# Kernel tuning notes

Hardware: AMD Instinct MI355X
Metric: run time of the kernel (lower is better)

## Reference

```python
import jax, jax.numpy as jnp
import numpy as np

DIM = 1024
N_HEADS = 16
HEAD_DIM = DIM // N_HEADS  # 64
HALF = HEAD_DIM // 2       # 32
DEPTH = 6
N_BRANCH = 2
NEG_INF = -1e9


def _rot_H(x, cos, sin, m):
    # H direction: adjacent-pair complex layout (..., HALF, 2)
    # x: [B,S,H,D], cos/sin: [HALF], m: [B,S] int
    B, S, H, D = x.shape
    xr = x.reshape(B, S, H, HALF, 2)
    re, im = xr[..., 0], xr[..., 1]
    re2 = re * cos - im * sin
    im2 = re * sin + im * cos
    rot = jnp.stack([re2, im2], axis=-1).reshape(B, S, H, D)
    return jnp.where((m != 0)[:, :, None, None], rot, x)


def _rot_B(x, cos, sin, m):
    # B direction: split-half complex layout (real = first half, imag = second half)
    re, im = x[..., :HALF], x[..., HALF:]
    re2 = re * cos - im * sin
    im2 = re * sin + im * cos
    rot = jnp.concatenate([re2, im2], axis=-1)
    return jnp.where((m != 0)[:, :, None, None], rot, x)


def _apply_rope_instructions(x, H_mask, B_mask, freqs_cos, freqs_sin):
    # Sequentially compose rotations per depth level, as in the torch loops.
    for i in range(DEPTH):
        x = _rot_H(x, freqs_cos[1], freqs_sin[1], H_mask[i])
        for b in range(N_BRANCH):
            x = _rot_B(x, freqs_cos[b + 1], freqs_sin[b + 1], B_mask[i, b])
    return x


def setup_inputs() -> dict:
    key = jax.random.key(0)
    ks = jax.random.split(key, 10)
    B, S = 2, 1024
    x = jax.random.normal(ks[0], (B, S, DIM), dtype=jnp.float32)
    masks = jax.random.randint(ks[1], (B, 1, S, S), 0, 2, dtype=jnp.int32)
    H_mask = jax.random.randint(ks[2], (DEPTH, B, S), 0, 2, dtype=jnp.int32)
    B_mask = jax.random.randint(ks[3], (DEPTH, N_BRANCH, B, S), 0, 2, dtype=jnp.int32)
    theta = jax.random.uniform(ks[4], (4, HALF), dtype=jnp.float32) * 2.0 * np.pi
    freqs_cos = jnp.cos(theta)
    freqs_sin = jnp.sin(theta)
    scale = 1.0 / np.sqrt(DIM)
    wq = jax.random.normal(ks[5], (DIM, DIM), dtype=jnp.float32) * scale
    wk = jax.random.normal(ks[6], (DIM, DIM), dtype=jnp.float32) * scale
    wv = jax.random.normal(ks[7], (DIM, DIM), dtype=jnp.float32) * scale
    wo = jax.random.normal(ks[8], (DIM, DIM), dtype=jnp.float32) * scale
    return {"x": x, "masks": masks, "H_mask": H_mask, "B_mask": B_mask,
            "freqs_cos": freqs_cos, "freqs_sin": freqs_sin,
            "wq": wq, "wk": wk, "wv": wv, "wo": wo}


def reference(x, masks, H_mask, B_mask, freqs_cos, freqs_sin, wq, wk, wv, wo):
    B, S, _ = x.shape
    xq = (x @ wq).reshape(B, S, N_HEADS, HEAD_DIM)
    xk = (x @ wk).reshape(B, S, N_HEADS, HEAD_DIM)
    xv = (x @ wv).reshape(B, S, N_HEADS, HEAD_DIM)
    xq = _apply_rope_instructions(xq, H_mask, B_mask, freqs_cos, freqs_sin)
    xk = _apply_rope_instructions(xk, H_mask, B_mask, freqs_cos, freqs_sin)
    scores = jnp.einsum('bqhd,bkhd->bhqk', xq, xk) / np.sqrt(HEAD_DIM)
    scores = jnp.where(masks == 0, NEG_INF, scores)
    probs = jax.nn.softmax(scores, axis=-1)
    out = jnp.einsum('bhqk,bkhd->bqhd', probs, xv).reshape(B, S, DIM)
    return out @ wo
```

## Files before the change

### kernel.cpp

```cpp
#include <hip/hip_runtime.h>

#define SLEN 1024
#define BATCH 2
#define DEPTH 6

typedef _Float16 h8 __attribute__((ext_vector_type(8)));
typedef float    f4 __attribute__((ext_vector_type(4)));
#define MF16(a, b, c) __builtin_amdgcn_mfma_f32_16x16x32_f16(a, b, c, 0, 0, 0)

#define SW(row, c) ((((c) ^ ((row) & 7))) * 8)

__device__ __forceinline__ void async_cp16(const _Float16* g, _Float16* l) {
  __builtin_amdgcn_global_load_lds(
      (const __attribute__((address_space(1))) void*)g,
      (__attribute__((address_space(3))) void*)l, 16, 0, 0);
}

__global__ __launch_bounds__(256) void prep(const float* __restrict__ x,
    const float* __restrict__ wq, const float* __restrict__ wk,
    const float* __restrict__ wv, const float* __restrict__ wo,
    const int* __restrict__ masks, _Float16* __restrict__ xh,
    _Float16* __restrict__ qt, _Float16* __restrict__ kt,
    _Float16* __restrict__ vt, _Float16* __restrict__ ot,
    unsigned int* __restrict__ mpk) {
  __shared__ _Float16 T[64][72];
  const int bid = blockIdx.x, t = threadIdx.x;
  if (bid < 1024) {
    int idx = (bid * 256 + t) * 8;
    float4 f0 = *(const float4*)(x + idx);
    float4 f1 = *(const float4*)(x + idx + 4);
    union { h8 v; _Float16 e[8]; } u;
    u.e[0] = (_Float16)f0.x; u.e[1] = (_Float16)f0.y;
    u.e[2] = (_Float16)f0.z; u.e[3] = (_Float16)f0.w;
    u.e[4] = (_Float16)f1.x; u.e[5] = (_Float16)f1.y;
    u.e[6] = (_Float16)f1.z; u.e[7] = (_Float16)f1.w;
    *(h8*)(xh + idx) = u.v;
  } else if (bid < 2048) {
    const int i = bid - 1024;
    const int wsel = i >> 8;
    const float* W = wsel == 0 ? wq : wsel == 1 ? wk : wsel == 2 ? wv : wo;
    _Float16* O = wsel == 0 ? qt : wsel == 1 ? kt : wsel == 2 ? vt : ot;
    const int k0 = ((i >> 4) & 15) * 64, n0 = (i & 15) * 64;
    const int rr = t >> 2, cs = (t & 3) * 16;
    #pragma unroll
    for (int j = 0; j < 4; ++j) {
      float4 f = *(const float4*)(W + (size_t)(k0 + rr) * 1024 + n0 + cs + j * 4);
      T[rr][cs + j * 4 + 0] = (_Float16)f.x;
      T[rr][cs + j * 4 + 1] = (_Float16)f.y;
      T[rr][cs + j * 4 + 2] = (_Float16)f.z;
      T[rr][cs + j * 4 + 3] = (_Float16)f.w;
    }
    __syncthreads();
    const int n = t >> 2, ks = (t & 3) * 16;
    union { h8 v; _Float16 e[8]; } u0, u1;
    #pragma unroll
    for (int j = 0; j < 8; ++j) { u0.e[j] = T[ks + j][n]; u1.e[j] = T[ks + 8 + j][n]; }
    *(h8*)(O + (size_t)(n0 + n) * 1024 + k0 + ks)     = u0.v;
    *(h8*)(O + (size_t)(n0 + n) * 1024 + k0 + ks + 8) = u1.v;
  } else {
    const int g = (bid - 2048) * 256 + t;
    const int row = g >> 5, w = g & 31;
    const int* m = masks + (size_t)row * 1024 + w * 32;
    unsigned int bits = 0;
    #pragma unroll
    for (int j4 = 0; j4 < 8; ++j4) {
      int4 mm = *(const int4*)(m + j4 * 4);
      if (mm.x) bits |= 1u << (j4 * 4 + 0);
      if (mm.y) bits |= 1u << (j4 * 4 + 1);
      if (mm.z) bits |= 1u << (j4 * 4 + 2);
      if (mm.w) bits |= 1u << (j4 * 4 + 3);
    }
    mpk[g] = bits;
  }
}

template <int TMODE, typename CT>
__device__ __forceinline__ void gemm16(const _Float16* __restrict__ A,
                                       const _Float16* __restrict__ Bt,
                                       CT* __restrict__ C,
                                       const int* __restrict__ Hm,
                                       const int* __restrict__ Bm,
                                       _Float16* __restrict__ SH,
                                       const float* __restrict__ FR) {
  _Float16* As = SH;
  _Float16* Bs = SH + 4096;
  const int t    = threadIdx.x;
  const int bm   = blockIdx.y * 64, bn = blockIdx.x * 128;
  const int w    = t >> 6, lane = t & 63;
  const int ln15 = lane & 15, quad = lane >> 4;
  const int wm   = (w >> 1) * 32, wn = (w & 1) * 64;

  const int srow8 = lane >> 3;
  const int sch   = (lane & 7) ^ srow8;
  const _Float16* agp = A  + (size_t)(bm + w * 16 + srow8) * 1024 + sch * 8;
  const _Float16* bgp = Bt + (size_t)(bn + w * 32 + srow8) * 1024 + sch * 8;

  f4 acc[2][4];
  #pragma unroll
  for (int i = 0; i < 2; ++i)
    #pragma unroll
    for (int j = 0; j < 4; ++j) acc[i][j] = (f4){0.f, 0.f, 0.f, 0.f};

  for (int k0 = 0; k0 < 1024; k0 += 64) {
    #pragma unroll
    for (int j = 0; j < 2; ++j)
      async_cp16(agp + k0 + j * 8192, As + w * 1024 + j * 512);
    #pragma unroll
    for (int j = 0; j < 4; ++j)
      async_cp16(bgp + k0 + j * 8192, Bs + w * 2048 + j * 512);
    __syncthreads();
    #pragma unroll
    for (int kk = 0; kk < 8; kk += 4) {
      h8 af[2], bf[4];
      #pragma unroll
      for (int i = 0; i < 2; ++i) {
        int row = wm + i * 16 + ln15;
        af[i] = *(const h8*)&As[row * 64 + SW(row, kk + quad)];
      }
      #pragma unroll
      for (int j = 0; j < 4; ++j) {
        int row = wn + j * 16 + ln15;
        bf[j] = *(const h8*)&Bs[row * 64 + SW(row, kk + quad)];
      }
      #pragma unroll
      for (int i = 0; i < 2; ++i)
        #pragma unroll
        for (int j = 0; j < 4; ++j)
          acc[i][j] = MF16(af[i], bf[j], acc[i][j]);
    }
    __syncthreads();
  }

  if (TMODE == 0) {
    #pragma unroll
    for (int i = 0; i < 2; ++i) {
      int row = bm + wm + i * 16 + quad * 4;
      #pragma unroll
      for (int r = 0; r < 4; ++r)
        #pragma unroll
        for (int j = 0; j < 4; ++j)
          C[(size_t)(row + r) * 1024 + bn + wn + j * 16 + ln15] = (CT)acc[i][j][r];
    }
  } else if (TMODE == 1) {
    #pragma unroll
    for (int i = 0; i < 2; ++i) {
      int m0 = bm + wm + i * 16 + quad * 4;
      #pragma unroll
      for (int r = 0; r < 4; ++r) {
        int m = m0 + r;
        size_t base = ((size_t)(m >> 10) * 1024) * 1024 + (m & 1023);
        #pragma unroll
        for (int j = 0; j < 4; ++j)
          C[base + (size_t)(bn + wn + j * 16 + ln15) * 1024] = (CT)acc[i][j][r];
      }
    }
  } else {
    _Float16* EP = SH;
    #pragma unroll
    for (int i = 0; i < 2; ++i)
      #pragma unroll
      for (int j = 0; j < 4; ++j) {
        int cl = wn + j * 16 + ln15;
        #pragma unroll
        for (int r = 0; r < 4; ++r) {
          int rl = wm + i * 16 + quad * 4 + r;
          EP[rl * 128 + (((cl >> 3) ^ (rl & 15)) << 3) + (cl & 7)] =
              (_Float16)acc[i][j][r];
        }
      }
    __syncthreads();
    const int row = t >> 2, head = (t >> 1) & 1, p = t & 1;
    const int bs = bm + row;
    const int r15 = row & 15;
    float vv[32];
    #pragma unroll
    for (int cc = 0; cc < 4; ++cc) {
      int lc = head * 8 + 2 * p + (cc & 1) + (cc >> 1) * 4;
      union { h8 v; _Float16 e[8]; } u;
      u.v = *(const h8*)&EP[row * 128 + (lc ^ r15) * 8];
      #pragma unroll
      for (int e = 0; e < 8; ++e) vv[cc * 8 + e] = (float)u.e[e];
    }
    #pragma unroll 1
    for (int d = 0; d < DEPTH; ++d) {
      if (Hm[d * (BATCH * SLEN) + bs] != 0) {
        #pragma unroll
        for (int jj = 0; jj < 8; ++jj) {
          int j0 = 8 * p + jj, j1 = 16 + 8 * p + jj;
          float re0 = vv[2 * jj], im0 = vv[2 * jj + 1];
          vv[2 * jj]     = re0 * FR[j0] - im0 * FR[32 + j0];
          vv[2 * jj + 1] = re0 * FR[32 + j0] + im0 * FR[j0];
          float re1 = vv[16 + 2 * jj], im1 = vv[17 + 2 * jj];
          vv[16 + 2 * jj] = re1 * FR[j1] - im1 * FR[32 + j1];
          vv[17 + 2 * jj] = re1 * FR[32 + j1] + im1 * FR[j1];
        }
      }
      if (Bm[(d * 2 + 0) * (BATCH * SLEN) + bs] != 0) {
        #pragma unroll
        for (int jj = 0; jj < 16; ++jj) {
          int j = 16 * p + jj;
          float re = vv[jj], im = vv[16 + jj];
          vv[jj]      = re * FR[j] - im * FR[32 + j];
          vv[16 + jj] = re * FR[32 + j] + im * FR[j];
        }
      }
      if (Bm[(d * 2 + 1) * (BATCH * SLEN) + bs] != 0) {
        #pragma unroll
        for (int jj = 0; jj < 16; ++jj) {
          int j = 16 * p + jj;
          float re = vv[jj], im = vv[16 + jj];
          vv[jj]      = re * FR[64 + j] - im * FR[96 + j];
          vv[16 + jj] = re * FR[96 + j] + im * FR[64 + j];
        }
      }
    }
    _Float16* dst = (_Float16*)C + (size_t)(bm + row) * 1024 + bn + head * 64;
    #pragma unroll
    for (int cc = 0; cc < 4; ++cc) {
      union { h8 v; _Float16 e[8]; } u;
      #pragma unroll
      for (int e = 0; e < 8; ++e) u.e[e] = (_Float16)vv[cc * 8 + e];
      int off = (cc < 2) ? (16 * p + cc * 8) : (32 + 16 * p + (cc - 2) * 8);
      *(h8*)(dst + off) = u.v;
    }
  }
}

__global__ __launch_bounds__(256) void gemm_qkv16(
    const _Float16* __restrict__ xh, const _Float16* __restrict__ qt,
    const _Float16* __restrict__ kt, const _Float16* __restrict__ vtw,
    _Float16* __restrict__ q, _Float16* __restrict__ k,
    _Float16* __restrict__ vth, const int* __restrict__ Hm,
    const int* __restrict__ Bm, const float* __restrict__ fc,
    const float* __restrict__ fs) {
  __shared__ _Float16 SH[12288];
  __shared__ float FR[128];
  if (blockIdx.z != 2 && threadIdx.x < 128) {
    int g = threadIdx.x & 31;
    FR[threadIdx.x] = (threadIdx.x < 32) ? fc[32 + g]
                    : (threadIdx.x < 64) ? fs[32 + g]
                    : (threadIdx.x < 96) ? fc[64 + g] : fs[64 + g];
  }
  if (blockIdx.z == 2)
    gemm16<1, _Float16>(xh, vtw, vth, nullptr, nullptr, SH, nullptr);
  else if (blockIdx.z == 1)
    gemm16<2, _Float16>(xh, kt, k, Hm, Bm, SH, FR);
  else
    gemm16<2, _Float16>(xh, qt, q, Hm, Bm, SH, FR);
}

__global__ __launch_bounds__(256) void gemm_o16(
    const _Float16* __restrict__ A, const _Float16* __restrict__ Bt,
    float* __restrict__ C) {
  __shared__ _Float16 SH[12288];
  gemm16<0, float>(A, Bt, C, nullptr, nullptr, SH, nullptr);
}

__global__ __launch_bounds__(256) void attn_mfma(const _Float16* __restrict__ qh,
    const _Float16* __restrict__ kh, const _Float16* __restrict__ vth,
    const unsigned int* __restrict__ mpk, _Float16* __restrict__ out) {
  __shared__ _Float16 Ks[2][64 * 64];
  __shared__ _Float16 Vs[2][64 * 64];
  __shared__ _Float16 QP[4][16][72];

  const int t    = threadIdx.x;
  const int w    = t >> 6, lane = t & 63;
  const int ln15 = lane & 15, quad = lane >> 4;

  const int bh = blockIdx.x & 31;
  const int s0 = (blockIdx.x >> 5) * 64;
  const int b = bh >> 4, h = bh & 15;
  const size_t qkbase = (size_t)b * (SLEN * 1024) + h * 64;
  const size_t vbase  = ((size_t)b * 1024 + h * 64) * SLEN;

  {
    const int srow = t >> 2, sc0 = (t & 3) * 16;
    const _Float16* src = qh + qkbase + (size_t)(s0 + srow) * 1024 + sc0;
    *(h8*)&QP[w][srow & 15][sc0]     = *(const h8*)src;
    *(h8*)&QP[w][srow & 15][sc0 + 8] = *(const h8*)(src + 8);
  }
  h8 aq0 = *(h8*)&QP[w][ln15][quad * 8];
  h8 aq1 = *(h8*)&QP[w][ln15][32 + quad * 8];

  const int srow8 = lane >> 3;
  const int sch   = (lane & 7) ^ srow8;
  const _Float16* kgp = kh + qkbase + (size_t)(w * 16 + srow8) * 1024 + sch * 8;
  const _Float16* vgp = vth + vbase + (size_t)(w * 16 + srow8) * 1024 + sch * 8;

  const unsigned int* mp = mpk + ((size_t)b * SLEN + s0 + w * 16 + quad * 4) * 32;

  float lrow[4] = {1e-30f, 1e-30f, 1e-30f, 1e-30f};
  f4 oacc[4];
  #pragma unroll
  for (int f = 0; f < 4; ++f) oacc[f] = (f4){0.f, 0.f, 0.f, 0.f};

  async_cp16(kgp,        &Ks[0][w * 1024]);
  async_cp16(kgp + 8192, &Ks[0][w * 1024 + 512]);
  async_cp16(vgp,        &Vs[0][w * 1024]);
  async_cp16(vgp + 8192, &Vs[0][w * 1024 + 512]);
  unsigned int w0[4], w1[4];
  #pragma unroll
  for (int r = 0; r < 4; ++r) { w0[r] = mp[r * 32]; w1[r] = mp[r * 32 + 1]; }
  __syncthreads();

  for (int c = 0; c < 16; ++c) {
    const int cur = c & 1;
    unsigned int nw0[4], nw1[4];
    if (c < 15) {
      const size_t ko = (size_t)((c + 1) * 64) * 1024;
      const int    vo = (c + 1) * 64;
      async_cp16(kgp + ko,        &Ks[cur ^ 1][w * 1024]);
      async_cp16(kgp + ko + 8192, &Ks[cur ^ 1][w * 1024 + 512]);
      async_cp16(vgp + vo,        &Vs[cur ^ 1][w * 1024]);
      async_cp16(vgp + vo + 8192, &Vs[cur ^ 1][w * 1024 + 512]);
      #pragma unroll
      for (int r = 0; r < 4; ++r) {
        nw0[r] = mp[r * 32 + (c + 1) * 2];
        nw1[r] = mp[r * 32 + (c + 1) * 2 + 1];
      }
    }

    f4 s[4];
    #pragma unroll
    for (int f = 0; f < 4; ++f) {
      int row = f * 16 + ln15;
      h8 bk0 = *(const h8*)&Ks[cur][row * 64 + SW(row, quad)];
      h8 bk1 = *(const h8*)&Ks[cur][row * 64 + SW(row, 4 + quad)];
      f4 acc = (f4){0.f, 0.f, 0.f, 0.f};
      acc = MF16(aq0, bk0, acc);
      acc = MF16(aq1, bk1, acc);
      s[f] = acc;
    }
    #pragma unroll
    for (int f = 0; f < 4; ++f) {
      const int col = f * 16 + ln15;
      #pragma unroll
      for (int r = 0; r < 4; ++r) {
        unsigned int wd = (col & 32) ? w1[r] : w0[r];
        float p = ((wd >> (col & 31)) & 1u)
                    ? __expf(s[f][r] * 0.125f - 3.0f) : 0.0f;
        lrow[r] += p;
        QP[w][quad * 4 + r][col] = (_Float16)p;
      }
    }
    h8 ap0 = *(h8*)&QP[w][ln15][quad * 8];
    h8 ap1 = *(h8*)&QP[w][ln15][32 + quad * 8];
    #pragma unroll
    for (int f = 0; f < 4; ++f) {
      int row = f * 16 + ln15;
      h8 bv0 = *(const h8*)&Vs[cur][row * 64 + SW(row, quad)];
      h8 bv1 = *(const h8*)&Vs[cur][row * 64 + SW(row, 4 + quad)];
      f4 o = oacc[f];
      o = MF16(ap0, bv0, o);
      o = MF16(ap1, bv1, o);
      oacc[f] = o;
    }
    if (c < 15) {
      #pragma unroll
      for (int r = 0; r < 4; ++r) { w0[r] = nw0[r]; w1[r] = nw1[r]; }
    }
    __syncthreads();
  }

  #pragma unroll
  for (int r = 0; r < 4; ++r) {
    float sm = lrow[r];
    sm += __shfl_xor(sm, 1);
    sm += __shfl_xor(sm, 2);
    sm += __shfl_xor(sm, 4);
    sm += __shfl_xor(sm, 8);
    lrow[r] = 1.0f / sm;
  }
  #pragma unroll
  for (int f = 0; f < 4; ++f)
    #pragma unroll
    for (int r = 0; r < 4; ++r)
      QP[w][quad * 4 + r][f * 16 + ln15] = (_Float16)(oacc[f][r] * lrow[r]);
  const int orow = lane >> 2, oseg = (lane & 3) * 16;
  _Float16* op = out + qkbase + (size_t)(s0 + w * 16 + orow) * 1024 + oseg;
  *(h8*)op       = *(h8*)&QP[w][orow][oseg];
  *(h8*)(op + 8) = *(h8*)&QP[w][orow][oseg + 8];
}

extern "C" void kernel_launch(void* const* d_in, const int* in_sizes, int n_in,
                              void* d_out, int out_size, void* d_ws, size_t ws_size,
                              hipStream_t stream) {
  const float* x     = (const float*)d_in[0];
  const int*   masks = (const int*)d_in[1];
  const int*   Hm    = (const int*)d_in[2];
  const int*   Bm    = (const int*)d_in[3];
  const float* fc    = (const float*)d_in[4];
  const float* fs    = (const float*)d_in[5];
  const float* wq    = (const float*)d_in[6];
  const float* wk    = (const float*)d_in[7];
  const float* wv    = (const float*)d_in[8];
  const float* wo    = (const float*)d_in[9];
  float* out = (float*)d_out;

  _Float16* xh   = (_Float16*)d_ws;
  _Float16* wqt  = xh + (1 << 21);
  _Float16* wkt  = wqt + (1 << 20);
  _Float16* wvt  = wkt + (1 << 20);
  _Float16* wot  = wvt + (1 << 20);
  _Float16* qhh  = wot + (1 << 20);
  _Float16* khh  = qhh + (1 << 21);
  _Float16* vth  = khh + (1 << 21);
  _Float16* aoh  = vth + (1 << 21);
  unsigned int* mpk = (unsigned int*)(aoh + (1 << 21));

  dim3 blk(256);
  prep<<<dim3(2304), blk, 0, stream>>>(x, wq, wk, wv, wo, masks,
                                       xh, wqt, wkt, wvt, wot, mpk);
  gemm_qkv16<<<dim3(8, 32, 3), blk, 0, stream>>>(xh, wqt, wkt, wvt,
                                                 qhh, khh, vth, Hm, Bm, fc, fs);
  attn_mfma<<<dim3(512), blk, 0, stream>>>(qhh, khh, vth, mpk, aoh);
  gemm_o16<<<dim3(8, 32), blk, 0, stream>>>(aoh, wot, out);
}
```

Before: 158.9 us.

## Switch attention to 32x32 MFMA with 2x2 wave split over query and key halves

Rewrites the attention kernel's inner loop to use 32x32x16 MFMA instead of 16x16x32. The four waves are arranged as a 2x2 grid over query-row halves and key-column halves, and the partial outputs and row sums are combined through LDS at the end. The aim is fewer MFMA issues and fewer LDS fragment loads per tile, plus better operand reuse. In exchange it adds a cross-wave reduction epilogue with extra LDS traffic and syncs, and each wave now holds 16 mask words in registers.

Result: slower. 163.1 us (+2.6%).

```diff
diff --git a/kernel.cpp b/kernel.cpp
--- a/kernel.cpp
+++ b/kernel.cpp
@@ -6,7 +6,9 @@
 
 typedef _Float16 h8 __attribute__((ext_vector_type(8)));
 typedef float    f4 __attribute__((ext_vector_type(4)));
+typedef float    f16f __attribute__((ext_vector_type(16)));
 #define MF16(a, b, c) __builtin_amdgcn_mfma_f32_16x16x32_f16(a, b, c, 0, 0, 0)
+#define MF32(a, b, c) __builtin_amdgcn_mfma_f32_32x32x16_f16(a, b, c, 0, 0, 0)
 
 #define SW(row, c) ((((c) ^ ((row) & 7))) * 8)
 
@@ -259,13 +261,15 @@
 __global__ __launch_bounds__(256) void attn_mfma(const _Float16* __restrict__ qh,
     const _Float16* __restrict__ kh, const _Float16* __restrict__ vth,
     const unsigned int* __restrict__ mpk, _Float16* __restrict__ out) {
-  __shared__ _Float16 Ks[2][64 * 64];
-  __shared__ _Float16 Vs[2][64 * 64];
-  __shared__ _Float16 QP[4][16][72];
+  __shared__ _Float16 Ks[2][4096];
+  __shared__ _Float16 Vs[2][4096];
+  __shared__ _Float16 PB[4][1280];
 
   const int t    = threadIdx.x;
   const int w    = t >> 6, lane = t & 63;
-  const int ln15 = lane & 15, quad = lane >> 4;
+  const int l31  = lane & 31, hh = lane >> 5;
+  const int qh32 = (w & 1) * 32;
+  const int kh32 = (w >> 1) * 32;
 
   const int bh = blockIdx.x & 31;
   const int s0 = (blockIdx.x >> 5) * 64;
@@ -274,38 +278,49 @@
   const size_t vbase  = ((size_t)b * 1024 + h * 64) * SLEN;
 
   {
-    const int srow = t >> 2, sc0 = (t & 3) * 16;
-    const _Float16* src = qh + qkbase + (size_t)(s0 + srow) * 1024 + sc0;
-    *(h8*)&QP[w][srow & 15][sc0]     = *(const h8*)src;
-    *(h8*)&QP[w][srow & 15][sc0 + 8] = *(const h8*)(src + 8);
-  }
-  h8 aq0 = *(h8*)&QP[w][ln15][quad * 8];
-  h8 aq1 = *(h8*)&QP[w][ln15][32 + quad * 8];
+    const int srow = t >> 2, c0 = (t & 3) * 2;
+    const _Float16* src = qh + qkbase + (size_t)(s0 + srow) * 1024 + c0 * 8;
+    h8 q0 = *(const h8*)src;
+    h8 q1 = *(const h8*)(src + 8);
+    *(h8*)&Ks[0][srow * 64 + SW(srow, c0)]     = q0;
+    *(h8*)&Ks[0][srow * 64 + SW(srow, c0 + 1)] = q1;
+  }
+  __syncthreads();
+  h8 qf[4];
+  #pragma unroll
+  for (int kg = 0; kg < 4; ++kg) {
+    int row = qh32 + l31;
+    qf[kg] = *(const h8*)&Ks[0][row * 64 + SW(row, kg * 2 + hh)];
+  }
+  __syncthreads();
 
   const int srow8 = lane >> 3;
   const int sch   = (lane & 7) ^ srow8;
   const _Float16* kgp = kh + qkbase + (size_t)(w * 16 + srow8) * 1024 + sch * 8;
   const _Float16* vgp = vth + vbase + (size_t)(w * 16 + srow8) * 1024 + sch * 8;
 
-  const unsigned int* mp = mpk + ((size_t)b * SLEN + s0 + w * 16 + quad * 4) * 32;
-
-  float lrow[4] = {1e-30f, 1e-30f, 1e-30f, 1e-30f};
-  f4 oacc[4];
-  #pragma unroll
-  for (int f = 0; f < 4; ++f) oacc[f] = (f4){0.f, 0.f, 0.f, 0.f};
+  const unsigned int* mp =
+      mpk + ((size_t)b * SLEN + s0 + qh32 + 4 * hh) * 32 + (kh32 >> 5);
+
+  float lrow[16];
+  #pragma unroll
+  for (int r = 0; r < 16; ++r) lrow[r] = 1e-30f;
+  f16f o0, o1;
+  #pragma unroll
+  for (int r = 0; r < 16; ++r) { o0[r] = 0.f; o1[r] = 0.f; }
 
   async_cp16(kgp,        &Ks[0][w * 1024]);
   async_cp16(kgp + 8192, &Ks[0][w * 1024 + 512]);
   async_cp16(vgp,        &Vs[0][w * 1024]);
   async_cp16(vgp + 8192, &Vs[0][w * 1024 + 512]);
-  unsigned int w0[4], w1[4];
-  #pragma unroll
-  for (int r = 0; r < 4; ++r) { w0[r] = mp[r * 32]; w1[r] = mp[r * 32 + 1]; }
+  unsigned int mw[16];
+  #pragma unroll
+  for (int r = 0; r < 16; ++r) mw[r] = mp[((r & 3) + 8 * (r >> 2)) * 32];
   __syncthreads();
 
   for (int c = 0; c < 16; ++c) {
     const int cur = c & 1;
-    unsigned int nw0[4], nw1[4];
+    unsigned int nmw[16];
     if (c < 15) {
       const size_t ko = (size_t)((c + 1) * 64) * 1024;
       const int    vo = (c + 1) * 64;
@@ -314,72 +329,82 @@
       async_cp16(vgp + vo,        &Vs[cur ^ 1][w * 1024]);
       async_cp16(vgp + vo + 8192, &Vs[cur ^ 1][w * 1024 + 512]);
       #pragma unroll
-      for (int r = 0; r < 4; ++r) {
-        nw0[r] = mp[r * 32 + (c + 1) * 2];
-        nw1[r] = mp[r * 32 + (c + 1) * 2 + 1];
-      }
-    }
-
-    f4 s[4];
-    #pragma unroll
-    for (int f = 0; f < 4; ++f) {
-      int row = f * 16 + ln15;
-      h8 bk0 = *(const h8*)&Ks[cur][row * 64 + SW(row, quad)];
-      h8 bk1 = *(const h8*)&Ks[cur][row * 64 + SW(row, 4 + quad)];
-      f4 acc = (f4){0.f, 0.f, 0.f, 0.f};
-      acc = MF16(aq0, bk0, acc);
-      acc = MF16(aq1, bk1, acc);
-      s[f] = acc;
-    }
-    #pragma unroll
-    for (int f = 0; f < 4; ++f) {
-      const int col = f * 16 + ln15;
-      #pragma unroll
-      for (int r = 0; r < 4; ++r) {
-        unsigned int wd = (col & 32) ? w1[r] : w0[r];
-        float p = ((wd >> (col & 31)) & 1u)
-                    ? __expf(s[f][r] * 0.125f - 3.0f) : 0.0f;
-        lrow[r] += p;
-        QP[w][quad * 4 + r][col] = (_Float16)p;
-      }
-    }
-    h8 ap0 = *(h8*)&QP[w][ln15][quad * 8];
-    h8 ap1 = *(h8*)&QP[w][ln15][32 + quad * 8];
-    #pragma unroll
-    for (int f = 0; f < 4; ++f) {
-      int row = f * 16 + ln15;
-      h8 bv0 = *(const h8*)&Vs[cur][row * 64 + SW(row, quad)];
-      h8 bv1 = *(const h8*)&Vs[cur][row * 64 + SW(row, 4 + quad)];
-      f4 o = oacc[f];
-      o = MF16(ap0, bv0, o);
-      o = MF16(ap1, bv1, o);
-      oacc[f] = o;
+      for (int r = 0; r < 16; ++r)
+        nmw[r] = mp[((r & 3) + 8 * (r >> 2)) * 32 + (c + 1) * 2];
+    }
+
+    f16f s;
+    #pragma unroll
+    for (int r = 0; r < 16; ++r) s[r] = 0.f;
+    #pragma unroll
+    for (int kg = 0; kg < 4; ++kg) {
+      int row = kh32 + l31;
+      h8 kf = *(const h8*)&Ks[cur][row * 64 + SW(row, kg * 2 + hh)];
+      s = MF32(qf[kg], kf, s);
+    }
+    #pragma unroll
+    for (int r = 0; r < 16; ++r) {
+      float p = ((mw[r] >> l31) & 1u)
+                  ? __expf(s[r] * 0.125f - 3.0f) : 0.0f;
+      lrow[r] += p;
+      PB[w][((r & 3) + 8 * (r >> 2) + 4 * hh) * 40 + l31] = (_Float16)p;
+    }
+    h8 pf0 = *(const h8*)&PB[w][l31 * 40 + hh * 8];
+    h8 pf1 = *(const h8*)&PB[w][l31 * 40 + 16 + hh * 8];
+    #pragma unroll
+    for (int dt = 0; dt < 2; ++dt) {
+      #pragma unroll
+      for (int kg2 = 0; kg2 < 2; ++kg2) {
+        int row = dt * 32 + l31;
+        h8 vf = *(const h8*)&Vs[cur][row * 64 + SW(row, (kh32 >> 3) + kg2 * 2 + hh)];
+        if (dt == 0) o0 = MF32(kg2 ? pf1 : pf0, vf, o0);
+        else         o1 = MF32(kg2 ? pf1 : pf0, vf, o1);
+      }
     }
     if (c < 15) {
       #pragma unroll
-      for (int r = 0; r < 4; ++r) { w0[r] = nw0[r]; w1[r] = nw1[r]; }
+      for (int r = 0; r < 16; ++r) mw[r] = nmw[r];
     }
     __syncthreads();
   }
 
   #pragma unroll
-  for (int r = 0; r < 4; ++r) {
-    float sm = lrow[r];
-    sm += __shfl_xor(sm, 1);
-    sm += __shfl_xor(sm, 2);
-    sm += __shfl_xor(sm, 4);
-    sm += __shfl_xor(sm, 8);
-    lrow[r] = 1.0f / sm;
-  }
-  #pragma unroll
-  for (int f = 0; f < 4; ++f)
-    #pragma unroll
-    for (int r = 0; r < 4; ++r)
-      QP[w][quad * 4 + r][f * 16 + ln15] = (_Float16)(oacc[f][r] * lrow[r]);
-  const int orow = lane >> 2, oseg = (lane & 3) * 16;
-  _Float16* op = out + qkbase + (size_t)(s0 + w * 16 + orow) * 1024 + oseg;
-  *(h8*)op       = *(h8*)&QP[w][orow][oseg];
-  *(h8*)(op + 8) = *(h8*)&QP[w][orow][oseg + 8];
+  for (int r = 0; r < 16; ++r) {
+    float v = lrow[r];
+    v += __shfl_xor(v, 1);
+    v += __shfl_xor(v, 2);
+    v += __shfl_xor(v, 4);
+    v += __shfl_xor(v, 8);
+    v += __shfl_xor(v, 16);
+    lrow[r] = v;
+  }
+  float* OB = (float*)&Ks[0][0];
+  float* LS = (float*)&PB[0][0];
+  if (kh32) {
+    #pragma unroll
+    for (int r = 0; r < 16; ++r) {
+      int row = qh32 + (r & 3) + 8 * (r >> 2) + 4 * hh;
+      OB[row * 64 + l31]      = o0[r];
+      OB[row * 64 + 32 + l31] = o1[r];
+      if (l31 == 0) LS[row] = lrow[r];
+    }
+  }
+  __syncthreads();
+  _Float16* OT = &Vs[0][0];
+  if (!kh32) {
+    #pragma unroll
+    for (int r = 0; r < 16; ++r) {
+      int row = qh32 + (r & 3) + 8 * (r >> 2) + 4 * hh;
+      float inv = 1.0f / (lrow[r] + LS[row]);
+      OT[row * 72 + l31]      = (_Float16)((o0[r] + OB[row * 64 + l31]) * inv);
+      OT[row * 72 + 32 + l31] = (_Float16)((o1[r] + OB[row * 64 + 32 + l31]) * inv);
+    }
+  }
+  __syncthreads();
+  const int orow = t >> 2, oseg = (t & 3) * 16;
+  _Float16* op = out + qkbase + (size_t)(s0 + orow) * 1024 + oseg;
+  *(h8*)op       = *(h8*)&OT[orow * 72 + oseg];
+  *(h8*)(op + 8) = *(h8*)&OT[orow * 72 + oseg + 8];
 }
 
 extern "C" void kernel_launch(void* const* d_in, const int* in_sizes, int n_in,
```
